# Kernel optimization log

Measured on AMD Instinct MI355X. Metric: run time of the kernel, lower is better.

Reference implementation:

```python
import jax, jax.numpy as jnp
from jax import lax
import numpy as np

DIM = 384
H = W = 32
B = 32
HALF = DIM // 2


def _parc(x, pe, w, b, axis):
    """Global circular depthwise conv along `axis` (2=H, 3=W). w: (C,1,kh,kw)."""
    x = x + pe
    k = x.shape[axis]
    if axis == 2:
        x_cat = jnp.concatenate([x, x[:, :, : k - 1, :]], axis=2)
    else:
        x_cat = jnp.concatenate([x, x[:, :, :, : k - 1]], axis=3)
    out = lax.conv_general_dilated(
        x_cat, w, window_strides=(1, 1), padding='VALID',
        dimension_numbers=('NCHW', 'OIHW', 'NCHW'),
        feature_group_count=x.shape[1])
    return out + b[None, :, None, None]


def setup_inputs() -> dict:
    key = jax.random.key(0)
    ks = jax.random.split(key, 12)
    std = 0.02
    return {
        'x': jax.random.normal(ks[0], (B, DIM, H, W), jnp.float32),
        'pe_h': std * jax.random.normal(ks[1], (1, HALF, H, 1), jnp.float32),
        'w_h': std * jax.random.normal(ks[2], (HALF, 1, H, 1), jnp.float32),
        'b_h': jnp.zeros((HALF,), jnp.float32),
        'pe_w': std * jax.random.normal(ks[3], (1, HALF, 1, W), jnp.float32),
        'w_w': std * jax.random.normal(ks[4], (HALF, 1, 1, W), jnp.float32),
        'b_w': jnp.zeros((HALF,), jnp.float32),
        'ln_w': jnp.ones((DIM,), jnp.float32),
        'ln_b': jnp.zeros((DIM,), jnp.float32),
        'w1': std * jax.random.normal(ks[5], (DIM, 4 * DIM), jnp.float32),
        'b1': jnp.zeros((4 * DIM,), jnp.float32),
        'w2': std * jax.random.normal(ks[6], (4 * DIM, DIM), jnp.float32),
        'b2': jnp.zeros((DIM,), jnp.float32),
        'gamma': 1e-6 * jnp.ones((DIM,), jnp.float32),
    }


def reference(x, pe_h, w_h, b_h, pe_w, w_w, b_w, ln_w, ln_b, w1, b1, w2, b2, gamma):
    inp = x
    half = x.shape[1] // 2
    x_h = _parc(x[:, :half], pe_h, w_h, b_h, axis=2)
    x_w = _parc(x[:, half:], pe_w, w_w, b_w, axis=3)
    y = jnp.concatenate([x_h, x_w], axis=1).transpose(0, 2, 3, 1)  # NHWC
    # LayerNorm over channels (eps=1e-6)
    mu = y.mean(-1, keepdims=True)
    var = ((y - mu) ** 2).mean(-1, keepdims=True)
    y = (y - mu) / jnp.sqrt(var + 1e-6) * ln_w + ln_b
    # inverted MLP: dim -> 4*dim -> dim with exact GELU
    y = jax.nn.gelu(jnp.dot(y, w1) + b1, approximate=False)
    y = jnp.dot(y, w2) + b2
    y = gamma * y
    return inp + y.transpose(0, 3, 1, 2)
```

## Files before the change

### kernel.cpp

```cpp
#include <hip/hip_runtime.h>


typedef __attribute__((ext_vector_type(8))) short short8;
typedef __attribute__((ext_vector_type(4))) float f32x4;
typedef __attribute__((ext_vector_type(16))) float f32x16;
typedef __attribute__((ext_vector_type(4))) int int4v;
typedef __attribute__((ext_vector_type(8))) int i32x8;

__device__ __forceinline__ float bf2f(unsigned short u) {
  union { unsigned int i; float f; } v; v.i = ((unsigned int)u) << 16; return v.f;
}
__device__ __forceinline__ unsigned short f2bf(float f) {
  union { float f; unsigned int i; } v; v.f = f;
  unsigned int r = v.i + 0x7FFFu + ((v.i >> 16) & 1u);
  return (unsigned short)(r >> 16);
}

#if defined(__has_builtin)
#if __has_builtin(__builtin_amdgcn_global_load_lds)
#define HAS_GLL 1
#endif
#endif
#ifndef HAS_GLL
#define HAS_GLL 0
#endif

#if HAS_GLL
__device__ __forceinline__ void gload16(const void* g, void* l) {
  __builtin_amdgcn_global_load_lds((const __attribute__((address_space(1))) void*)g,
                                   (__attribute__((address_space(3))) void*)l, 16, 0, 0);
}
#else
__device__ __forceinline__ void gload16(const void* g, void* l) {
  *(f32x4*)l = *(const f32x4*)g;
}
#endif

template <int N>
__device__ __forceinline__ void wait_vm() {
  asm volatile("s_waitcnt vmcnt(%0)" :: "n"(N) : "memory");
}
__device__ __forceinline__ void barrier_raw() {
  __builtin_amdgcn_s_barrier();
  __builtin_amdgcn_sched_barrier(0);
}

__device__ __forceinline__ float fast_gelu(float h) {
  const float e = __builtin_amdgcn_exp2f(-2.4554005f * h);
  return h * __builtin_amdgcn_rcpf(1.f + e);
}

__device__ __forceinline__ int pk4(float a, float b, float c, float d) {
  int r = __builtin_amdgcn_cvt_pk_fp8_f32(a, b, 0, false);
  return __builtin_amdgcn_cvt_pk_fp8_f32(c, d, r, true);
}

#define SCL1 0x7F7F7F7F

__device__ __forceinline__ int packed_off(int row, int kc) {
  return ((row >> 5) << 11) + ((kc & 1) << 10) + ((kc >> 1) << 9) + ((row & 31) << 4);
}

__global__ __launch_bounds__(256) void prep_kernel(
    const float* __restrict__ w1, const float* __restrict__ w2,
    char* __restrict__ w1p, char* __restrict__ w2p,
    const float* __restrict__ x,
    const float* __restrict__ pe_h, const float* __restrict__ w_h, const float* __restrict__ b_h,
    const float* __restrict__ pe_w, const float* __restrict__ w_w, const float* __restrict__ b_w,
    unsigned short* __restrict__ convout) {
  const int t = threadIdx.x;
  int bid = blockIdx.x;
  if (bid < 60) {
    float v[64];
    if (bid < 36) {
      const int kt = bid % 6, hg = bid / 6;
      const int h = hg * 256 + t;
      #pragma unroll
      for (int k = 0; k < 64; ++k) v[k] = w1[(size_t)(kt * 64 + k) * 1536 + h];
      char* base = w1p + (size_t)kt * 1536 * 64;
      #pragma unroll
      for (int k0 = 0; k0 < 64; k0 += 4)
        *(int*)(base + packed_off(h, k0 >> 4) + (k0 & 12)) =
            pk4(v[k0], v[k0 + 1], v[k0 + 2], v[k0 + 3]);
    } else {
      const int kt = bid - 36;
      for (int c = t; c < 384; c += 256) {
        #pragma unroll
        for (int k = 0; k < 64; ++k) v[k] = w2[(size_t)(kt * 64 + k) * 384 + c];
        char* base = w2p + (size_t)kt * 384 * 64;
        #pragma unroll
        for (int k0 = 0; k0 < 64; k0 += 4)
          *(int*)(base + packed_off(c, k0 >> 4) + (k0 & 12)) =
              pk4(v[k0], v[k0 + 1], v[k0 + 2], v[k0 + 3]);
      }
    }
    return;
  }
  bid -= 60;
  __shared__ float wt_s[8][32], pe_s[8][32], pc_s[8][32];
  const int b = bid / 48, g = bid % 48;
  const int c0 = g << 3;
  const bool ish = (c0 < 192);
  const int cl = t >> 5, q = t & 31;
  {
    const int c = c0 + cl;
    if (ish) { wt_s[cl][q] = w_h[(c << 5) + q];           pe_s[cl][q] = pe_h[(c << 5) + q]; }
    else     { const int cc = c - 192;
               wt_s[cl][q] = w_w[(cc << 5) + q];          pe_s[cl][q] = pe_w[(cc << 5) + q]; }
  }
  __syncthreads();
  {
    float s = ish ? b_h[c0 + cl] : b_w[c0 + cl - 192];
    #pragma unroll
    for (int i = 0; i < 32; ++i) s += pe_s[cl][(q + i) & 31] * wt_s[cl][i];
    pc_s[cl][q] = s;
  }
  __syncthreads();
  const float* xp = x + ((size_t)(b * 384 + c0 + cl) << 10);
  float col[32];
  if (ish) {
    #pragma unroll
    for (int j = 0; j < 32; ++j) col[j] = xp[(j << 5) + q];
  } else {
    const float* rp = xp + (q << 5);
    #pragma unroll
    for (int j4 = 0; j4 < 8; ++j4) {
      f32x4 v = *(const f32x4*)&rp[j4 << 2];
      col[j4 * 4 + 0] = v[0]; col[j4 * 4 + 1] = v[1];
      col[j4 * 4 + 2] = v[2]; col[j4 * 4 + 3] = v[3];
    }
  }
  float wr[32];
  #pragma unroll
  for (int i = 0; i < 32; ++i) wr[i] = wt_s[cl][i];
  float o[32];
  #pragma unroll
  for (int oo = 0; oo < 32; ++oo) o[oo] = pc_s[cl][oo];
  #pragma unroll
  for (int i = 0; i < 32; ++i)
    #pragma unroll
    for (int oo = 0; oo < 32; ++oo)
      o[oo] = fmaf(col[(oo + i) & 31], wr[i], o[oo]);
  unsigned short* op = convout + ((size_t)(b * 384 + c0 + cl) << 10);
  if (ish) {
    #pragma unroll
    for (int oo = 0; oo < 32; ++oo) op[(oo << 5) + q] = f2bf(o[oo]);
  } else {
    #pragma unroll
    for (int j8 = 0; j8 < 4; ++j8) {
      short8 p;
      #pragma unroll
      for (int j = 0; j < 8; ++j) p[j] = (short)f2bf(o[j8 * 8 + j]);
      *(short8*)&op[(q << 5) + j8 * 8] = p;
    }
  }
}

__global__ __launch_bounds__(256) void ln_fused_kernel(
    const unsigned short* __restrict__ conv, char* __restrict__ ylnp,
    const float* __restrict__ ln_w, const float* __restrict__ ln_b) {
  __shared__ unsigned short tile[384][72];
  __shared__ float lws[384], lbs[384];
  __shared__ float ps[4][64], pq[4][64];
  __shared__ float mus[64], rss[64];
  const int t = threadIdx.x;
  const int pb = blockIdx.x;
  const int b = pb >> 4;
  const int hw0 = (pb & 15) << 6;
  for (int i = t; i < 384; i += 256) { lws[i] = ln_w[i]; lbs[i] = ln_b[i]; }
  #pragma unroll
  for (int i = 0; i < 12; ++i) {
    const int idx = t + i * 256;
    const int c = idx >> 3, j = idx & 7;
    short8 v = *(const short8*)(conv + (((size_t)(b * 384 + c)) << 10) + hw0 + j * 8);
    *(short8*)&tile[c][j * 8] = v;
  }
  __syncthreads();
  {
    const int l = t & 63, qt = t >> 6;
    float s = 0.f, ss = 0.f;
    #pragma unroll
    for (int k = 0; k < 96; ++k) {
      const float v = bf2f(tile[qt * 96 + k][l]);
      s += v; ss = fmaf(v, v, ss);
    }
    ps[qt][l] = s; pq[qt][l] = ss;
  }
  __syncthreads();
  if (t < 64) {
    const float st = ps[0][t] + ps[1][t] + ps[2][t] + ps[3][t];
    const float sq = pq[0][t] + pq[1][t] + pq[2][t] + pq[3][t];
    const float m = st * (1.f / 384.f);
    const float var = sq * (1.f / 384.f) - m * m;
    mus[t] = m; rss[t] = rsqrtf(var + 1e-6f);
  }
  __syncthreads();
  const int l = t & 63, kc = t >> 6;
  const int px = pb * 64 + l;
  const float m = mus[l], r = rss[l];
  #pragma unroll
  for (int kt = 0; kt < 6; ++kt) {
    const int c0 = kt * 64 + kc * 16;
    float ov[16];
    #pragma unroll
    for (int e = 0; e < 16; ++e) {
      const float v = bf2f(tile[c0 + e][l]);
      ov[e] = (v - m) * r * lws[c0 + e] + lbs[c0 + e];
    }
    int4v d;
    d[0] = pk4(ov[0],  ov[1],  ov[2],  ov[3]);
    d[1] = pk4(ov[4],  ov[5],  ov[6],  ov[7]);
    d[2] = pk4(ov[8],  ov[9],  ov[10], ov[11]);
    d[3] = pk4(ov[12], ov[13], ov[14], ov[15]);
    *(int4v*)(ylnp + (size_t)kt * 32768 * 64 + packed_off(px, kc)) = d;
  }
}

template <int EPI, int KDIM, int AROWS, int NWN>
__global__ __launch_bounds__(NWN * 128, 4) void gemm_kernel(
    const char* __restrict__ Ab, const char* __restrict__ Bb,
    char* __restrict__ Hout8, const float* __restrict__ bias,
    const float* __restrict__ gamma, const float* __restrict__ xres,
    float* __restrict__ out, int px0, int bstride, int boff, int hstride,
    int nwg, int nx) {
  extern __shared__ char lds[];
  constexpr int BM = 128;
  constexpr int BN = NWN * 64;
  constexpr int THREADS = NWN * 128;
  constexpr int NB = 3;
  constexpr int NT = KDIM / 64;
  constexpr int SLOT = BN * 64;
  constexpr int BCH = BN * 4 / THREADS;
  static_assert(BCH == 2, "vmcnt schedule assumes 2 B-ops/thread");
  const int tid = threadIdx.x;
  const int lane = tid & 63;
  const int wid = tid >> 6;
  const int wm = wid / NWN;
  const int wn = wid % NWN;
  const int lane31 = lane & 31;
  const int kh = lane >> 5;
  const int bid = blockIdx.x;
  const int q = nwg >> 3, r = nwg & 7;
  const int xcd = bid & 7, idx = bid >> 3;
  const int lg = (xcd < r ? xcd * (q + 1) : r * (q + 1) + (xcd - r) * q) + idx;
  const int xb = lg % nx, yb = lg / nx;
  const int arow0 = xb * BM;
  const int brow0 = yb * BN;

  f32x16 acc[2][2] = {};

  const char* aglob = Ab + ((size_t)(arow0 + wm * 64)) * 64 + (kh << 9) + (lane31 << 4);
  int bbase[2];
  #pragma unroll
  for (int n = 0; n < 2; ++n)
    bbase[n] = ((wn * 2 + n) << 11) + (kh << 9) + (lane31 << 4);

  auto stageB = [&](int tile) {
    char* sl = lds + (tile % NB) * SLOT;
    const char* bsrc = Bb + ((size_t)tile * bstride + boff + brow0) * 64;
    #pragma unroll
    for (int i = 0; i < BCH; ++i)
      gload16(bsrc + (i * THREADS + tid) * 16, sl + (i * THREADS + tid) * 16);
  };
  auto loadA = [&](int t, i32x8& f0, i32x8& f1) {
    const char* p = aglob + (size_t)t * (size_t)(AROWS * 64);
    int4v q0 = *(const int4v*)(p);
    int4v q1 = *(const int4v*)(p + 1024);
    int4v q2 = *(const int4v*)(p + 2048);
    int4v q3 = *(const int4v*)(p + 3072);
    f0[0]=q0[0]; f0[1]=q0[1]; f0[2]=q0[2]; f0[3]=q0[3];
    f0[4]=q1[0]; f0[5]=q1[1]; f0[6]=q1[2]; f0[7]=q1[3];
    f1[0]=q2[0]; f1[1]=q2[1]; f1[2]=q2[2]; f1[3]=q2[3];
    f1[4]=q3[0]; f1[5]=q3[1]; f1[6]=q3[2]; f1[7]=q3[3];
  };
  auto readB = [&](int t, i32x8 bv[2]) {
    const char* slp = lds + (t % NB) * SLOT;
    #pragma unroll
    for (int n = 0; n < 2; ++n) {
      int4v p0 = *(const int4v*)(slp + bbase[n]);
      int4v p1 = *(const int4v*)(slp + bbase[n] + 1024);
      bv[n][0]=p0[0]; bv[n][1]=p0[1]; bv[n][2]=p0[2]; bv[n][3]=p0[3];
      bv[n][4]=p1[0]; bv[n][5]=p1[1]; bv[n][6]=p1[2]; bv[n][7]=p1[3];
    }
  };
  auto mfma4 = [&](i32x8& a0, i32x8& a1, i32x8 bv[2]) {
    __builtin_amdgcn_s_setprio(1);
    acc[0][0] = __builtin_amdgcn_mfma_scale_f32_32x32x64_f8f6f4(
        a0, bv[0], acc[0][0], 0, 0, 0, SCL1, 0, SCL1);
    acc[0][1] = __builtin_amdgcn_mfma_scale_f32_32x32x64_f8f6f4(
        a0, bv[1], acc[0][1], 0, 0, 0, SCL1, 0, SCL1);
    acc[1][0] = __builtin_amdgcn_mfma_scale_f32_32x32x64_f8f6f4(
        a1, bv[0], acc[1][0], 0, 0, 0, SCL1, 0, SCL1);
    acc[1][1] = __builtin_amdgcn_mfma_scale_f32_32x32x64_f8f6f4(
        a1, bv[1], acc[1][1], 0, 0, 0, SCL1, 0, SCL1);
    __builtin_amdgcn_s_setprio(0);
  };

  i32x8 aA0, aA1, aB0, aB1;
  loadA(0, aA0, aA1);
  stageB(0);
  stageB(1);
  wait_vm<2>();
  barrier_raw();

  int t = 0;
  #pragma unroll 1
  for (; t + 3 < NT; t += 2) {
    {
      i32x8 bv[2]; readB(t, bv);
      loadA(t + 1, aB0, aB1);
      stageB(t + 2);
      mfma4(aA0, aA1, bv);
      wait_vm<2>();
      barrier_raw();
    }
    {
      i32x8 bv[2]; readB(t + 1, bv);
      loadA(t + 2, aA0, aA1);
      stageB(t + 3);
      mfma4(aB0, aB1, bv);
      wait_vm<2>();
      barrier_raw();
    }
  }
  {
    i32x8 bv[2]; readB(t, bv);
    loadA(t + 1, aB0, aB1);
    mfma4(aA0, aA1, bv);
    wait_vm<0>();
    barrier_raw();
  }
  {
    i32x8 bv[2]; readB(t + 1, bv);
    mfma4(aB0, aB1, bv);
  }

  if (EPI == 0) {
    #pragma unroll
    for (int fm = 0; fm < 2; ++fm) {
      const int wmf = wm * 2 + fm;
      const int kt2 = (arow0 >> 6) + (wmf >> 1);
      #pragma unroll
      for (int G = 0; G < 4; ++G) {
        const int hbyte = ((wmf & 1) << 5) + 8 * G + 4 * kh;
        const int hglob = arow0 + (wmf << 5) + 8 * G + 4 * kh;
        const float c0 = bias[hglob + 0], c1 = bias[hglob + 1];
        const float c2 = bias[hglob + 2], c3 = bias[hglob + 3];
        const int kc = hbyte >> 4, sub = hbyte & 15;
        #pragma unroll
        for (int n = 0; n < 2; ++n) {
          const int px = brow0 + wn * 64 + n * 32 + lane31;
          const int d = pk4(fast_gelu(acc[fm][n][4 * G + 0] + c0),
                            fast_gelu(acc[fm][n][4 * G + 1] + c1),
                            fast_gelu(acc[fm][n][4 * G + 2] + c2),
                            fast_gelu(acc[fm][n][4 * G + 3] + c3));
          *(int*)(Hout8 + (size_t)kt2 * hstride * 64 + packed_off(px, kc) + sub) = d;
        }
      }
    }
  } else {
    #pragma unroll
    for (int fm = 0; fm < 2; ++fm) {
      const int wmf = wm * 2 + fm;
      #pragma unroll
      for (int G = 0; G < 4; ++G) {
        #pragma unroll
        for (int j = 0; j < 4; ++j) {
          const int c = arow0 + (wmf << 5) + 8 * G + 4 * kh + j;
          const float gv = gamma[c];
          const float bvv = bias[c];
          #pragma unroll
          for (int n = 0; n < 2; ++n) {
            const int px = px0 + brow0 + wn * 64 + n * 32 + lane31;
            const int bb = px >> 10, hw = px & 1023;
            const size_t oi = (((size_t)(bb * 384 + c)) << 10) + hw;
            out[oi] = xres[oi] + gv * (acc[fm][n][4 * G + j] + bvv);
          }
        }
      }
    }
  }
}

extern "C" void kernel_launch(void* const* d_in, const int* in_sizes, int n_in,
                              void* d_out, int out_size, void* d_ws, size_t ws_size,
                              hipStream_t stream) {
  (void)in_sizes; (void)n_in; (void)out_size;
  const float* x     = (const float*)d_in[0];
  const float* pe_h  = (const float*)d_in[1];
  const float* w_h   = (const float*)d_in[2];
  const float* b_h   = (const float*)d_in[3];
  const float* pe_w  = (const float*)d_in[4];
  const float* w_w   = (const float*)d_in[5];
  const float* b_w   = (const float*)d_in[6];
  const float* ln_w  = (const float*)d_in[7];
  const float* ln_b  = (const float*)d_in[8];
  const float* w1    = (const float*)d_in[9];
  const float* b1    = (const float*)d_in[10];
  const float* w2    = (const float*)d_in[11];
  const float* b2    = (const float*)d_in[12];
  const float* gamma = (const float*)d_in[13];
  float* out = (float*)d_out;
  char* ws = (char*)d_ws;

  char*           W1P  = ws;
  char*           W2P  = ws + 589824;
  char*           YLNP = ws + 1441792;
  unsigned short* CONV = (unsigned short*)(ws + 14024704);
  char*           HID  = ws + 14024704;

  int G = 32;
  while (G > 2) {
    size_t hid = (size_t)G * 1572864ull;
    size_t need = 14024704ull + (hid > 25165824ull ? hid : 25165824ull);
    if (need <= ws_size) break;
    G -= 2;
  }

  constexpr int LDS1 = 256 * 64 * 3;
  constexpr int LDS2 = 128 * 64 * 3;

  prep_kernel<<<dim3(1596), dim3(256), 0, stream>>>(
      w1, w2, W1P, W2P, x, pe_h, w_h, b_h, pe_w, w_w, b_w, CONV);
  ln_fused_kernel<<<dim3(512), dim3(256), 0, stream>>>(CONV, YLNP, ln_w, ln_b);
  for (int i0 = 0; i0 < 32; i0 += G) {
    const int gi = (32 - i0 < G) ? (32 - i0) : G;
    const int Mpx = gi * 1024;
    {
      const int nwg = 12 * (Mpx / 256);
      gemm_kernel<0, 384, 1536, 4><<<dim3(nwg), dim3(512), LDS1, stream>>>(
          W1P, YLNP, HID, b1, nullptr, nullptr, nullptr,
          0, 32768, i0 * 1024, Mpx, nwg, 12);
    }
    {
      const int nwg = 3 * (Mpx / 128);
      gemm_kernel<1, 1536, 384, 2><<<dim3(nwg), dim3(256), LDS2, stream>>>(
          W2P, HID, nullptr, b2, gamma, x, out, i0 * 1024, Mpx, 0, 0, nwg, 3);
    }
  }
}
```

Before: 98.79 us.

## Split GEMM kernel; preload full K panel for GEMM1 with 128x128 tiles

The shared templated GEMM is split into two specialised kernels. GEMM1 now uses 256-thread workgroups with 128x128 tiles and loads the whole K=384 B panel (six 8 KB slices) into LDS up front. Its main loop then runs without per-step barriers or a rotating triple buffer. This removes synchronisation overhead in the short-K GEMM and doubles the number of workgroups, in exchange for no overlap between the initial load and compute and for reloading the A operand across more blocks. GEMM2 is functionally unchanged apart from cleaner vector assembly.

Result: no change. 97.46 us (-1.4%).

```diff
diff --git a/kernel.cpp b/kernel.cpp
--- a/kernel.cpp
+++ b/kernel.cpp
@@ -14,6 +14,9 @@
   union { float f; unsigned int i; } v; v.f = f;
   unsigned int r = v.i + 0x7FFFu + ((v.i >> 16) & 1u);
   return (unsigned short)(r >> 16);
+}
+__device__ __forceinline__ i32x8 combine(int4v lo, int4v hi) {
+  return __builtin_shufflevector(lo, hi, 0, 1, 2, 3, 4, 5, 6, 7);
 }
 
 #if defined(__has_builtin)
@@ -216,27 +219,17 @@
   }
 }
 
-template <int EPI, int KDIM, int AROWS, int NWN>
-__global__ __launch_bounds__(NWN * 128, 4) void gemm_kernel(
+template <int KDIM, int AROWS>
+__global__ __launch_bounds__(256, 3) void gemm1_kernel(
     const char* __restrict__ Ab, const char* __restrict__ Bb,
     char* __restrict__ Hout8, const float* __restrict__ bias,
-    const float* __restrict__ gamma, const float* __restrict__ xres,
-    float* __restrict__ out, int px0, int bstride, int boff, int hstride,
-    int nwg, int nx) {
+    int bstride, int boff, int hstride, int nwg, int nx) {
   extern __shared__ char lds[];
-  constexpr int BM = 128;
-  constexpr int BN = NWN * 64;
-  constexpr int THREADS = NWN * 128;
-  constexpr int NB = 3;
   constexpr int NT = KDIM / 64;
-  constexpr int SLOT = BN * 64;
-  constexpr int BCH = BN * 4 / THREADS;
-  static_assert(BCH == 2, "vmcnt schedule assumes 2 B-ops/thread");
   const int tid = threadIdx.x;
   const int lane = tid & 63;
   const int wid = tid >> 6;
-  const int wm = wid / NWN;
-  const int wn = wid % NWN;
+  const int wm = wid >> 1, wn = wid & 1;
   const int lane31 = lane & 31;
   const int kh = lane >> 5;
   const int bid = blockIdx.x;
@@ -244,55 +237,122 @@
   const int xcd = bid & 7, idx = bid >> 3;
   const int lg = (xcd < r ? xcd * (q + 1) : r * (q + 1) + (xcd - r) * q) + idx;
   const int xb = lg % nx, yb = lg / nx;
-  const int arow0 = xb * BM;
-  const int brow0 = yb * BN;
+  const int arow0 = xb * 128;
+  const int brow0 = yb * 128;
+
+  #pragma unroll
+  for (int tt = 0; tt < NT; ++tt) {
+    const char* bsrc = Bb + ((size_t)tt * bstride + boff + brow0) * 64;
+    gload16(bsrc + tid * 16,          lds + tt * 8192 + tid * 16);
+    gload16(bsrc + (256 + tid) * 16,  lds + tt * 8192 + (256 + tid) * 16);
+  }
+  const char* aglob = Ab + ((size_t)(arow0 + wm * 64)) * 64 + (kh << 9) + (lane31 << 4);
+  const int bb0 = ((wn * 2 + 0) << 11) + (kh << 9) + (lane31 << 4);
+  const int bb1 = ((wn * 2 + 1) << 11) + (kh << 9) + (lane31 << 4);
+  wait_vm<0>();
+  barrier_raw();
 
   f32x16 acc[2][2] = {};
+  #pragma unroll 3
+  for (int t = 0; t < NT; ++t) {
+    const char* slp = lds + t * 8192;
+    i32x8 bv0 = combine(*(const int4v*)(slp + bb0), *(const int4v*)(slp + bb0 + 1024));
+    i32x8 bv1 = combine(*(const int4v*)(slp + bb1), *(const int4v*)(slp + bb1 + 1024));
+    const char* p = aglob + (size_t)t * (size_t)(AROWS * 64);
+    i32x8 a0 = combine(*(const int4v*)(p),        *(const int4v*)(p + 1024));
+    i32x8 a1 = combine(*(const int4v*)(p + 2048), *(const int4v*)(p + 3072));
+    __builtin_amdgcn_s_setprio(1);
+    acc[0][0] = __builtin_amdgcn_mfma_scale_f32_32x32x64_f8f6f4(
+        a0, bv0, acc[0][0], 0, 0, 0, SCL1, 0, SCL1);
+    acc[0][1] = __builtin_amdgcn_mfma_scale_f32_32x32x64_f8f6f4(
+        a0, bv1, acc[0][1], 0, 0, 0, SCL1, 0, SCL1);
+    acc[1][0] = __builtin_amdgcn_mfma_scale_f32_32x32x64_f8f6f4(
+        a1, bv0, acc[1][0], 0, 0, 0, SCL1, 0, SCL1);
+    acc[1][1] = __builtin_amdgcn_mfma_scale_f32_32x32x64_f8f6f4(
+        a1, bv1, acc[1][1], 0, 0, 0, SCL1, 0, SCL1);
+    __builtin_amdgcn_s_setprio(0);
+  }
+
+  #pragma unroll
+  for (int fm = 0; fm < 2; ++fm) {
+    const int wmf = wm * 2 + fm;
+    const int kt2 = (arow0 >> 6) + (wmf >> 1);
+    #pragma unroll
+    for (int G = 0; G < 4; ++G) {
+      const int hbyte = ((wmf & 1) << 5) + 8 * G + 4 * kh;
+      const int hglob = arow0 + (wmf << 5) + 8 * G + 4 * kh;
+      const float c0 = bias[hglob + 0], c1 = bias[hglob + 1];
+      const float c2 = bias[hglob + 2], c3 = bias[hglob + 3];
+      const int kc = hbyte >> 4, sub = hbyte & 15;
+      #pragma unroll
+      for (int n = 0; n < 2; ++n) {
+        const int px = brow0 + wn * 64 + n * 32 + lane31;
+        const int d = pk4(fast_gelu(acc[fm][n][4 * G + 0] + c0),
+                          fast_gelu(acc[fm][n][4 * G + 1] + c1),
+                          fast_gelu(acc[fm][n][4 * G + 2] + c2),
+                          fast_gelu(acc[fm][n][4 * G + 3] + c3));
+        *(int*)(Hout8 + (size_t)kt2 * hstride * 64 + packed_off(px, kc) + sub) = d;
+      }
+    }
+  }
+}
+
+template <int KDIM, int AROWS>
+__global__ __launch_bounds__(256, 4) void gemm2_kernel(
+    const char* __restrict__ Ab, const char* __restrict__ Bb,
+    const float* __restrict__ bias, const float* __restrict__ gamma,
+    const float* __restrict__ xres, float* __restrict__ out,
+    int px0, int bstride, int boff, int nwg, int nx) {
+  extern __shared__ char lds[];
+  constexpr int NB = 3;
+  constexpr int NT = KDIM / 64;
+  constexpr int SLOT = 128 * 64;
+  const int tid = threadIdx.x;
+  const int lane = tid & 63;
+  const int wid = tid >> 6;
+  const int wm = wid >> 1, wn = wid & 1;
+  const int lane31 = lane & 31;
+  const int kh = lane >> 5;
+  const int bid = blockIdx.x;
+  const int q = nwg >> 3, r = nwg & 7;
+  const int xcd = bid & 7, idx = bid >> 3;
+  const int lg = (xcd < r ? xcd * (q + 1) : r * (q + 1) + (xcd - r) * q) + idx;
+  const int xb = lg % nx, yb = lg / nx;
+  const int arow0 = xb * 128;
+  const int brow0 = yb * 128;
+
+  f32x16 acc[2][2] = {};
 
   const char* aglob = Ab + ((size_t)(arow0 + wm * 64)) * 64 + (kh << 9) + (lane31 << 4);
-  int bbase[2];
-  #pragma unroll
-  for (int n = 0; n < 2; ++n)
-    bbase[n] = ((wn * 2 + n) << 11) + (kh << 9) + (lane31 << 4);
+  const int bb0 = ((wn * 2 + 0) << 11) + (kh << 9) + (lane31 << 4);
+  const int bb1 = ((wn * 2 + 1) << 11) + (kh << 9) + (lane31 << 4);
 
   auto stageB = [&](int tile) {
     char* sl = lds + (tile % NB) * SLOT;
     const char* bsrc = Bb + ((size_t)tile * bstride + boff + brow0) * 64;
-    #pragma unroll
-    for (int i = 0; i < BCH; ++i)
-      gload16(bsrc + (i * THREADS + tid) * 16, sl + (i * THREADS + tid) * 16);
+    gload16(bsrc + tid * 16,         sl + tid * 16);
+    gload16(bsrc + (256 + tid) * 16, sl + (256 + tid) * 16);
   };
   auto loadA = [&](int t, i32x8& f0, i32x8& f1) {
     const char* p = aglob + (size_t)t * (size_t)(AROWS * 64);
-    int4v q0 = *(const int4v*)(p);
-    int4v q1 = *(const int4v*)(p + 1024);
-    int4v q2 = *(const int4v*)(p + 2048);
-    int4v q3 = *(const int4v*)(p + 3072);
-    f0[0]=q0[0]; f0[1]=q0[1]; f0[2]=q0[2]; f0[3]=q0[3];
-    f0[4]=q1[0]; f0[5]=q1[1]; f0[6]=q1[2]; f0[7]=q1[3];
-    f1[0]=q2[0]; f1[1]=q2[1]; f1[2]=q2[2]; f1[3]=q2[3];
-    f1[4]=q3[0]; f1[5]=q3[1]; f1[6]=q3[2]; f1[7]=q3[3];
+    f0 = combine(*(const int4v*)(p),        *(const int4v*)(p + 1024));
+    f1 = combine(*(const int4v*)(p + 2048), *(const int4v*)(p + 3072));
   };
-  auto readB = [&](int t, i32x8 bv[2]) {
+  auto readB = [&](int t, i32x8& bv0, i32x8& bv1) {
     const char* slp = lds + (t % NB) * SLOT;
-    #pragma unroll
-    for (int n = 0; n < 2; ++n) {
-      int4v p0 = *(const int4v*)(slp + bbase[n]);
-      int4v p1 = *(const int4v*)(slp + bbase[n] + 1024);
-      bv[n][0]=p0[0]; bv[n][1]=p0[1]; bv[n][2]=p0[2]; bv[n][3]=p0[3];
-      bv[n][4]=p1[0]; bv[n][5]=p1[1]; bv[n][6]=p1[2]; bv[n][7]=p1[3];
-    }
+    bv0 = combine(*(const int4v*)(slp + bb0), *(const int4v*)(slp + bb0 + 1024));
+    bv1 = combine(*(const int4v*)(slp + bb1), *(const int4v*)(slp + bb1 + 1024));
   };
-  auto mfma4 = [&](i32x8& a0, i32x8& a1, i32x8 bv[2]) {
+  auto mfma4 = [&](i32x8& a0, i32x8& a1, i32x8& bv0, i32x8& bv1) {
     __builtin_amdgcn_s_setprio(1);
     acc[0][0] = __builtin_amdgcn_mfma_scale_f32_32x32x64_f8f6f4(
-        a0, bv[0], acc[0][0], 0, 0, 0, SCL1, 0, SCL1);
+        a0, bv0, acc[0][0], 0, 0, 0, SCL1, 0, SCL1);
     acc[0][1] = __builtin_amdgcn_mfma_scale_f32_32x32x64_f8f6f4(
-        a0, bv[1], acc[0][1], 0, 0, 0, SCL1, 0, SCL1);
+        a0, bv1, acc[0][1], 0, 0, 0, SCL1, 0, SCL1);
     acc[1][0] = __builtin_amdgcn_mfma_scale_f32_32x32x64_f8f6f4(
-        a1, bv[0], acc[1][0], 0, 0, 0, SCL1, 0, SCL1);
+        a1, bv0, acc[1][0], 0, 0, 0, SCL1, 0, SCL1);
     acc[1][1] = __builtin_amdgcn_mfma_scale_f32_32x32x64_f8f6f4(
-        a1, bv[1], acc[1][1], 0, 0, 0, SCL1, 0, SCL1);
+        a1, bv1, acc[1][1], 0, 0, 0, SCL1, 0, SCL1);
     __builtin_amdgcn_s_setprio(0);
   };
 
@@ -307,75 +367,50 @@
   #pragma unroll 1
   for (; t + 3 < NT; t += 2) {
     {
-      i32x8 bv[2]; readB(t, bv);
+      i32x8 bv0, bv1; readB(t, bv0, bv1);
       loadA(t + 1, aB0, aB1);
       stageB(t + 2);
-      mfma4(aA0, aA1, bv);
+      mfma4(aA0, aA1, bv0, bv1);
       wait_vm<2>();
       barrier_raw();
     }
     {
-      i32x8 bv[2]; readB(t + 1, bv);
+      i32x8 bv0, bv1; readB(t + 1, bv0, bv1);
       loadA(t + 2, aA0, aA1);
       stageB(t + 3);
-      mfma4(aB0, aB1, bv);
+      mfma4(aB0, aB1, bv0, bv1);
       wait_vm<2>();
       barrier_raw();
     }
   }
   {
-    i32x8 bv[2]; readB(t, bv);
+    i32x8 bv0, bv1; readB(t, bv0, bv1);
     loadA(t + 1, aB0, aB1);
-    mfma4(aA0, aA1, bv);
+    mfma4(aA0, aA1, bv0, bv1);
     wait_vm<0>();
     barrier_raw();
   }
   {
-    i32x8 bv[2]; readB(t + 1, bv);
-    mfma4(aB0, aB1, bv);
-  }
-
-  if (EPI == 0) {
-    #pragma unroll
-    for (int fm = 0; fm < 2; ++fm) {
-      const int wmf = wm * 2 + fm;
-      const int kt2 = (arow0 >> 6) + (wmf >> 1);
+    i32x8 bv0, bv1; readB(t + 1, bv0, bv1);
+    mfma4(aB0, aB1, bv0, bv1);
+  }
+
+  #pragma unroll
+  for (int fm = 0; fm < 2; ++fm) {
+    const int wmf = wm * 2 + fm;
+    #pragma unroll
+    for (int G = 0; G < 4; ++G) {
       #pragma unroll
-      for (int G = 0; G < 4; ++G) {
-        const int hbyte = ((wmf & 1) << 5) + 8 * G + 4 * kh;
-        const int hglob = arow0 + (wmf << 5) + 8 * G + 4 * kh;
-        const float c0 = bias[hglob + 0], c1 = bias[hglob + 1];
-        const float c2 = bias[hglob + 2], c3 = bias[hglob + 3];
-        const int kc = hbyte >> 4, sub = hbyte & 15;
+      for (int j = 0; j < 4; ++j) {
+        const int c = arow0 + (wmf << 5) + 8 * G + 4 * kh + j;
+        const float gv = gamma[c];
+        const float bvv = bias[c];
         #pragma unroll
         for (int n = 0; n < 2; ++n) {
-          const int px = brow0 + wn * 64 + n * 32 + lane31;
-          const int d = pk4(fast_gelu(acc[fm][n][4 * G + 0] + c0),
-                            fast_gelu(acc[fm][n][4 * G + 1] + c1),
-                            fast_gelu(acc[fm][n][4 * G + 2] + c2),
-                            fast_gelu(acc[fm][n][4 * G + 3] + c3));
-          *(int*)(Hout8 + (size_t)kt2 * hstride * 64 + packed_off(px, kc) + sub) = d;
-        }
-      }
-    }
-  } else {
-    #pragma unroll
-    for (int fm = 0; fm < 2; ++fm) {
-      const int wmf = wm * 2 + fm;
-      #pragma unroll
-      for (int G = 0; G < 4; ++G) {
-        #pragma unroll
-        for (int j = 0; j < 4; ++j) {
-          const int c = arow0 + (wmf << 5) + 8 * G + 4 * kh + j;
-          const float gv = gamma[c];
-          const float bvv = bias[c];
-          #pragma unroll
-          for (int n = 0; n < 2; ++n) {
-            const int px = px0 + brow0 + wn * 64 + n * 32 + lane31;
-            const int bb = px >> 10, hw = px & 1023;
-            const size_t oi = (((size_t)(bb * 384 + c)) << 10) + hw;
-            out[oi] = xres[oi] + gv * (acc[fm][n][4 * G + j] + bvv);
-          }
+          const int px = px0 + brow0 + wn * 64 + n * 32 + lane31;
+          const int bb = px >> 10, hw = px & 1023;
+          const size_t oi = (((size_t)(bb * 384 + c)) << 10) + hw;
+          out[oi] = xres[oi] + gv * (acc[fm][n][4 * G + j] + bvv);
         }
       }
     }
@@ -417,7 +452,7 @@
     G -= 2;
   }
 
-  constexpr int LDS1 = 256 * 64 * 3;
+  constexpr int LDS1 = 6 * 8192;
   constexpr int LDS2 = 128 * 64 * 3;
 
   prep_kernel<<<dim3(1596), dim3(256), 0, stream>>>(
@@ -427,15 +462,14 @@
     const int gi = (32 - i0 < G) ? (32 - i0) : G;
     const int Mpx = gi * 1024;
     {
-      const int nwg = 12 * (Mpx / 256);
-      gemm_kernel<0, 384, 1536, 4><<<dim3(nwg), dim3(512), LDS1, stream>>>(
-          W1P, YLNP, HID, b1, nullptr, nullptr, nullptr,
-          0, 32768, i0 * 1024, Mpx, nwg, 12);
+      const int nwg = 12 * (Mpx / 128);
+      gemm1_kernel<384, 1536><<<dim3(nwg), dim3(256), LDS1, stream>>>(
+          W1P, YLNP, HID, b1, 32768, i0 * 1024, Mpx, nwg, 12);
     }
     {
       const int nwg = 3 * (Mpx / 128);
-      gemm_kernel<1, 1536, 384, 2><<<dim3(nwg), dim3(256), LDS2, stream>>>(
-          W2P, HID, nullptr, b2, gamma, x, out, i0 * 1024, Mpx, 0, 0, nwg, 3);
-    }
-  }
-}
+      gemm2_kernel<1536, 384><<<dim3(nwg), dim3(256), LDS2, stream>>>(
+          W2P, HID, b2, gamma, x, out, i0 * 1024, Mpx, 0, nwg, 3);
+    }
+  }
+}
```

## Fuse both MLP GEMMs into one kernel keeping hidden activations in LDS

Applied to the files above, without the earlier changes.

Replaces the two separate FP8 GEMM launches, which round-trip the 1536-wide hidden activation through global memory, with a single kernel. Each block takes 64 pixels, stages their LayerNorm output in LDS, computes the hidden GELU tile into LDS, then runs the second GEMM from LDS and writes the residual output. This removes the hidden-tensor write and read plus one launch. In exchange, weights are read straight from global memory (L2) with no LDS staging or software pipelining, LDS use per block is large (about 120 KB), which limits occupancy, and the grid is only 512 blocks.

Result: faster. 95.17 us (-3.7%).

```diff
diff --git a/kernel.cpp b/kernel.cpp
--- a/kernel.cpp
+++ b/kernel.cpp
@@ -15,6 +15,10 @@
   unsigned int r = v.i + 0x7FFFu + ((v.i >> 16) & 1u);
   return (unsigned short)(r >> 16);
 }
+__device__ __forceinline__ i32x8 combine(int4v lo, int4v hi) {
+  return __builtin_shufflevector(lo, hi, 0, 1, 2, 3, 4, 5, 6, 7);
+}
+__device__ __forceinline__ int4v ld16(const char* p) { return *(const int4v*)p; }
 
 #if defined(__has_builtin)
 #if __has_builtin(__builtin_amdgcn_global_load_lds)
@@ -216,167 +220,119 @@
   }
 }
 
-template <int EPI, int KDIM, int AROWS, int NWN>
-__global__ __launch_bounds__(NWN * 128, 4) void gemm_kernel(
-    const char* __restrict__ Ab, const char* __restrict__ Bb,
-    char* __restrict__ Hout8, const float* __restrict__ bias,
+__global__ __launch_bounds__(512, 2) void fused_mlp_kernel(
+    const char* __restrict__ W1P, const char* __restrict__ W2P,
+    const char* __restrict__ YLNP,
+    const float* __restrict__ b1, const float* __restrict__ b2,
     const float* __restrict__ gamma, const float* __restrict__ xres,
-    float* __restrict__ out, int px0, int bstride, int boff, int hstride,
-    int nwg, int nx) {
+    float* __restrict__ out) {
   extern __shared__ char lds[];
-  constexpr int BM = 128;
-  constexpr int BN = NWN * 64;
-  constexpr int THREADS = NWN * 128;
-  constexpr int NB = 3;
-  constexpr int NT = KDIM / 64;
-  constexpr int SLOT = BN * 64;
-  constexpr int BCH = BN * 4 / THREADS;
-  static_assert(BCH == 2, "vmcnt schedule assumes 2 B-ops/thread");
   const int tid = threadIdx.x;
   const int lane = tid & 63;
   const int wid = tid >> 6;
-  const int wm = wid / NWN;
-  const int wn = wid % NWN;
   const int lane31 = lane & 31;
   const int kh = lane >> 5;
-  const int bid = blockIdx.x;
-  const int q = nwg >> 3, r = nwg & 7;
-  const int xcd = bid & 7, idx = bid >> 3;
-  const int lg = (xcd < r ? xcd * (q + 1) : r * (q + 1) + (xcd - r) * q) + idx;
-  const int xb = lg % nx, yb = lg / nx;
-  const int arow0 = xb * BM;
-  const int brow0 = yb * BN;
-
-  f32x16 acc[2][2] = {};
-
-  const char* aglob = Ab + ((size_t)(arow0 + wm * 64)) * 64 + (kh << 9) + (lane31 << 4);
-  int bbase[2];
-  #pragma unroll
-  for (int n = 0; n < 2; ++n)
-    bbase[n] = ((wn * 2 + n) << 11) + (kh << 9) + (lane31 << 4);
-
-  auto stageB = [&](int tile) {
-    char* sl = lds + (tile % NB) * SLOT;
-    const char* bsrc = Bb + ((size_t)tile * bstride + boff + brow0) * 64;
-    #pragma unroll
-    for (int i = 0; i < BCH; ++i)
-      gload16(bsrc + (i * THREADS + tid) * 16, sl + (i * THREADS + tid) * 16);
-  };
-  auto loadA = [&](int t, i32x8& f0, i32x8& f1) {
-    const char* p = aglob + (size_t)t * (size_t)(AROWS * 64);
-    int4v q0 = *(const int4v*)(p);
-    int4v q1 = *(const int4v*)(p + 1024);
-    int4v q2 = *(const int4v*)(p + 2048);
-    int4v q3 = *(const int4v*)(p + 3072);
-    f0[0]=q0[0]; f0[1]=q0[1]; f0[2]=q0[2]; f0[3]=q0[3];
-    f0[4]=q1[0]; f0[5]=q1[1]; f0[6]=q1[2]; f0[7]=q1[3];
-    f1[0]=q2[0]; f1[1]=q2[1]; f1[2]=q2[2]; f1[3]=q2[3];
-    f1[4]=q3[0]; f1[5]=q3[1]; f1[6]=q3[2]; f1[7]=q3[3];
-  };
-  auto readB = [&](int t, i32x8 bv[2]) {
-    const char* slp = lds + (t % NB) * SLOT;
-    #pragma unroll
-    for (int n = 0; n < 2; ++n) {
-      int4v p0 = *(const int4v*)(slp + bbase[n]);
-      int4v p1 = *(const int4v*)(slp + bbase[n] + 1024);
-      bv[n][0]=p0[0]; bv[n][1]=p0[1]; bv[n][2]=p0[2]; bv[n][3]=p0[3];
-      bv[n][4]=p1[0]; bv[n][5]=p1[1]; bv[n][6]=p1[2]; bv[n][7]=p1[3];
-    }
-  };
-  auto mfma4 = [&](i32x8& a0, i32x8& a1, i32x8 bv[2]) {
-    __builtin_amdgcn_s_setprio(1);
-    acc[0][0] = __builtin_amdgcn_mfma_scale_f32_32x32x64_f8f6f4(
-        a0, bv[0], acc[0][0], 0, 0, 0, SCL1, 0, SCL1);
-    acc[0][1] = __builtin_amdgcn_mfma_scale_f32_32x32x64_f8f6f4(
-        a0, bv[1], acc[0][1], 0, 0, 0, SCL1, 0, SCL1);
-    acc[1][0] = __builtin_amdgcn_mfma_scale_f32_32x32x64_f8f6f4(
-        a1, bv[0], acc[1][0], 0, 0, 0, SCL1, 0, SCL1);
-    acc[1][1] = __builtin_amdgcn_mfma_scale_f32_32x32x64_f8f6f4(
-        a1, bv[1], acc[1][1], 0, 0, 0, SCL1, 0, SCL1);
-    __builtin_amdgcn_s_setprio(0);
-  };
-
-  i32x8 aA0, aA1, aB0, aB1;
-  loadA(0, aA0, aA1);
-  stageB(0);
-  stageB(1);
-  wait_vm<2>();
+  const int px0 = blockIdx.x << 6;
+  char* hl = lds + 24576;
+
+  #pragma unroll
+  for (int i = 0; i < 3; ++i) {
+    const int idx = i * 512 + tid;
+    const int kt = idx >> 8;
+    const int off = (idx & 255) << 4;
+    gload16(YLNP + (size_t)kt * 2097152 + ((size_t)px0 << 6) + off,
+            lds + kt * 4096 + off);
+  }
+  wait_vm<0>();
   barrier_raw();
 
-  int t = 0;
+  const int frkb = (kh << 9) + (lane31 << 4);
   #pragma unroll 1
-  for (; t + 3 < NT; t += 2) {
-    {
-      i32x8 bv[2]; readB(t, bv);
-      loadA(t + 1, aB0, aB1);
-      stageB(t + 2);
-      mfma4(aA0, aA1, bv);
-      wait_vm<2>();
-      barrier_raw();
-    }
-    {
-      i32x8 bv[2]; readB(t + 1, bv);
-      loadA(t + 2, aA0, aA1);
-      stageB(t + 3);
-      mfma4(aB0, aB1, bv);
-      wait_vm<2>();
-      barrier_raw();
-    }
-  }
-  {
-    i32x8 bv[2]; readB(t, bv);
-    loadA(t + 1, aB0, aB1);
-    mfma4(aA0, aA1, bv);
-    wait_vm<0>();
-    barrier_raw();
-  }
-  {
-    i32x8 bv[2]; readB(t + 1, bv);
-    mfma4(aB0, aB1, bv);
-  }
-
-  if (EPI == 0) {
+  for (int sc = 0; sc < 3; ++sc) {
+    const int hb = wid * 192 + sc * 64;
+    const char* ag = W1P + (hb << 6) + frkb;
+    f32x16 acc[2][2] = {};
+    #pragma unroll
+    for (int t = 0; t < 6; ++t) {
+      const char* p = ag + (size_t)t * 98304;
+      i32x8 a0 = combine(ld16(p),        ld16(p + 1024));
+      i32x8 a1 = combine(ld16(p + 2048), ld16(p + 3072));
+      const char* bt = lds + t * 4096 + frkb;
+      i32x8 bv0 = combine(ld16(bt),        ld16(bt + 1024));
+      i32x8 bv1 = combine(ld16(bt + 2048), ld16(bt + 3072));
+      __builtin_amdgcn_s_setprio(1);
+      acc[0][0] = __builtin_amdgcn_mfma_scale_f32_32x32x64_f8f6f4(
+          a0, bv0, acc[0][0], 0, 0, 0, SCL1, 0, SCL1);
+      acc[0][1] = __builtin_amdgcn_mfma_scale_f32_32x32x64_f8f6f4(
+          a0, bv1, acc[0][1], 0, 0, 0, SCL1, 0, SCL1);
+      acc[1][0] = __builtin_amdgcn_mfma_scale_f32_32x32x64_f8f6f4(
+          a1, bv0, acc[1][0], 0, 0, 0, SCL1, 0, SCL1);
+      acc[1][1] = __builtin_amdgcn_mfma_scale_f32_32x32x64_f8f6f4(
+          a1, bv1, acc[1][1], 0, 0, 0, SCL1, 0, SCL1);
+      __builtin_amdgcn_s_setprio(0);
+    }
     #pragma unroll
     for (int fm = 0; fm < 2; ++fm) {
-      const int wmf = wm * 2 + fm;
-      const int kt2 = (arow0 >> 6) + (wmf >> 1);
       #pragma unroll
       for (int G = 0; G < 4; ++G) {
-        const int hbyte = ((wmf & 1) << 5) + 8 * G + 4 * kh;
-        const int hglob = arow0 + (wmf << 5) + 8 * G + 4 * kh;
-        const float c0 = bias[hglob + 0], c1 = bias[hglob + 1];
-        const float c2 = bias[hglob + 2], c3 = bias[hglob + 3];
+        const int h = hb + fm * 32 + 8 * G + 4 * kh;
+        const float c0 = b1[h], c1 = b1[h + 1], c2 = b1[h + 2], c3 = b1[h + 3];
+        const int kt2 = h >> 6;
+        const int hbyte = h & 63;
         const int kc = hbyte >> 4, sub = hbyte & 15;
         #pragma unroll
         for (int n = 0; n < 2; ++n) {
-          const int px = brow0 + wn * 64 + n * 32 + lane31;
+          const int px = n * 32 + lane31;
           const int d = pk4(fast_gelu(acc[fm][n][4 * G + 0] + c0),
                             fast_gelu(acc[fm][n][4 * G + 1] + c1),
                             fast_gelu(acc[fm][n][4 * G + 2] + c2),
                             fast_gelu(acc[fm][n][4 * G + 3] + c3));
-          *(int*)(Hout8 + (size_t)kt2 * hstride * 64 + packed_off(px, kc) + sub) = d;
+          *(int*)(hl + kt2 * 4096 + packed_off(px, kc) + sub) = d;
         }
       }
     }
-  } else {
-    #pragma unroll
-    for (int fm = 0; fm < 2; ++fm) {
-      const int wmf = wm * 2 + fm;
-      #pragma unroll
-      for (int G = 0; G < 4; ++G) {
-        #pragma unroll
-        for (int j = 0; j < 4; ++j) {
-          const int c = arow0 + (wmf << 5) + 8 * G + 4 * kh + j;
-          const float gv = gamma[c];
-          const float bvv = bias[c];
-          #pragma unroll
-          for (int n = 0; n < 2; ++n) {
-            const int px = px0 + brow0 + wn * 64 + n * 32 + lane31;
-            const int bb = px >> 10, hw = px & 1023;
-            const size_t oi = (((size_t)(bb * 384 + c)) << 10) + hw;
-            out[oi] = xres[oi] + gv * (acc[fm][n][4 * G + j] + bvv);
-          }
-        }
+  }
+  asm volatile("s_waitcnt lgkmcnt(0)" ::: "memory");
+  barrier_raw();
+
+  const int pfrag = wid & 1;
+  const int cg3 = (wid >> 1) * 3;
+  const char* ag2 = W2P + (cg3 << 11) + frkb;
+  const int bboff = (pfrag << 11) + frkb;
+  f32x16 acc0 = {}, acc1 = {}, acc2 = {};
+  #pragma unroll 2
+  for (int t = 0; t < 24; ++t) {
+    const char* bt = hl + t * 4096 + bboff;
+    i32x8 bv = combine(ld16(bt), ld16(bt + 1024));
+    const char* p = ag2 + (size_t)t * 24576;
+    i32x8 a0 = combine(ld16(p),        ld16(p + 1024));
+    i32x8 a1 = combine(ld16(p + 2048), ld16(p + 3072));
+    i32x8 a2 = combine(ld16(p + 4096), ld16(p + 5120));
+    __builtin_amdgcn_s_setprio(1);
+    acc0 = __builtin_amdgcn_mfma_scale_f32_32x32x64_f8f6f4(
+        a0, bv, acc0, 0, 0, 0, SCL1, 0, SCL1);
+    acc1 = __builtin_amdgcn_mfma_scale_f32_32x32x64_f8f6f4(
+        a1, bv, acc1, 0, 0, 0, SCL1, 0, SCL1);
+    acc2 = __builtin_amdgcn_mfma_scale_f32_32x32x64_f8f6f4(
+        a2, bv, acc2, 0, 0, 0, SCL1, 0, SCL1);
+    __builtin_amdgcn_s_setprio(0);
+  }
+
+  const int px = px0 + pfrag * 32 + lane31;
+  const int bb = px >> 10, hw = px & 1023;
+  #pragma unroll
+  for (int j = 0; j < 3; ++j) {
+    const f32x16& aj = (j == 0) ? acc0 : (j == 1) ? acc1 : acc2;
+    const int cbase = (cg3 + j) * 32;
+    #pragma unroll
+    for (int G = 0; G < 4; ++G) {
+      #pragma unroll
+      for (int jj = 0; jj < 4; ++jj) {
+        const int c = cbase + 8 * G + 4 * kh + jj;
+        const float gv = gamma[c];
+        const float bvv = b2[c];
+        const size_t oi = (((size_t)(bb * 384 + c)) << 10) + hw;
+        out[oi] = xres[oi] + gv * (aj[4 * G + jj] + bvv);
       }
     }
   }
@@ -385,7 +341,7 @@
 extern "C" void kernel_launch(void* const* d_in, const int* in_sizes, int n_in,
                               void* d_out, int out_size, void* d_ws, size_t ws_size,
                               hipStream_t stream) {
-  (void)in_sizes; (void)n_in; (void)out_size;
+  (void)in_sizes; (void)n_in; (void)out_size; (void)ws_size;
   const float* x     = (const float*)d_in[0];
   const float* pe_h  = (const float*)d_in[1];
   const float* w_h   = (const float*)d_in[2];
@@ -407,35 +363,14 @@
   char*           W2P  = ws + 589824;
   char*           YLNP = ws + 1441792;
   unsigned short* CONV = (unsigned short*)(ws + 14024704);
-  char*           HID  = ws + 14024704;
-
-  int G = 32;
-  while (G > 2) {
-    size_t hid = (size_t)G * 1572864ull;
-    size_t need = 14024704ull + (hid > 25165824ull ? hid : 25165824ull);
-    if (need <= ws_size) break;
-    G -= 2;
-  }
-
-  constexpr int LDS1 = 256 * 64 * 3;
-  constexpr int LDS2 = 128 * 64 * 3;
+
+  constexpr int LDSF = 24576 + 98304;
+  (void)hipFuncSetAttribute((const void*)fused_mlp_kernel,
+                            hipFuncAttributeMaxDynamicSharedMemorySize, LDSF);
 
   prep_kernel<<<dim3(1596), dim3(256), 0, stream>>>(
       w1, w2, W1P, W2P, x, pe_h, w_h, b_h, pe_w, w_w, b_w, CONV);
   ln_fused_kernel<<<dim3(512), dim3(256), 0, stream>>>(CONV, YLNP, ln_w, ln_b);
-  for (int i0 = 0; i0 < 32; i0 += G) {
-    const int gi = (32 - i0 < G) ? (32 - i0) : G;
-    const int Mpx = gi * 1024;
-    {
-      const int nwg = 12 * (Mpx / 256);
-      gemm_kernel<0, 384, 1536, 4><<<dim3(nwg), dim3(512), LDS1, stream>>>(
-          W1P, YLNP, HID, b1, nullptr, nullptr, nullptr,
-          0, 32768, i0 * 1024, Mpx, nwg, 12);
-    }
-    {
-      const int nwg = 3 * (Mpx / 128);
-      gemm_kernel<1, 1536, 384, 2><<<dim3(nwg), dim3(256), LDS2, stream>>>(
-          W2P, HID, nullptr, b2, gamma, x, out, i0 * 1024, Mpx, 0, 0, nwg, 3);
-    }
-  }
-}
+  fused_mlp_kernel<<<dim3(512), dim3(512), LDSF, stream>>>(
+      W1P, W2P, YLNP, b1, b2, gamma, x, out);
+}
```
